# Optimization experiments

Measured on AMD Instinct MI355X. Metric: run time of the kernel, lower is better.

## Reference

```python
import jax, jax.numpy as jnp
import numpy as np

FLOW_NUM = 2048
H = 64  # lstm_output_dim
NOISE_DIM = 3


def _w(key, shape, s=0.08):
    return (jax.random.normal(key, shape, dtype=jnp.float32) * s)


def setup_inputs() -> dict:
    key = jax.random.key(0)
    ks = jax.random.split(key, 20)
    d = {
        "noise": jax.random.normal(ks[0], (FLOW_NUM, NOISE_DIM), dtype=jnp.float32),
        "w_ih0": _w(ks[1], (4 * H, NOISE_DIM)),
        "w_hh0": _w(ks[2], (4 * H, H)),
        "b_ih0": _w(ks[3], (4 * H,)),
        "b_hh0": _w(ks[4], (4 * H,)),
        "w_ih1": _w(ks[5], (4 * H, H)),
        "w_hh1": _w(ks[6], (4 * H, H)),
        "b_ih1": _w(ks[7], (4 * H,)),
        "b_hh1": _w(ks[8], (4 * H,)),
        "w_ih2": _w(ks[9], (4 * H, H)),
        "w_hh2": _w(ks[10], (4 * H, H)),
        "b_ih2": _w(ks[11], (4 * H,)),
        "b_hh2": _w(ks[12], (4 * H,)),
        "fc1_w": _w(ks[13], (32, H)),
        "fc1_b": _w(ks[14], (32,)),
        "fc2_w": _w(ks[15], (16, 32)),
        "fc2_b": _w(ks[16], (16,)),
        "fc3_w": _w(ks[17], (3, 16)),
        "fc3_b": _w(ks[18], (3,)),
        "flow_length": 500,
    }
    return d


def _lstm_cell(x, h, c, w_ih, w_hh, b_ih, b_hh):
    # PyTorch gate order: input, forget, cell(g), output
    gates = x @ w_ih.T + h @ w_hh.T + (b_ih + b_hh)
    i, f, g, o = jnp.split(gates, 4, axis=-1)
    c_new = jax.nn.sigmoid(f) * c + jax.nn.sigmoid(i) * jnp.tanh(g)
    h_new = jax.nn.sigmoid(o) * jnp.tanh(c_new)
    return h_new, c_new


def reference(noise, w_ih0, w_hh0, b_ih0, b_hh0,
              w_ih1, w_hh1, b_ih1, b_hh1,
              w_ih2, w_hh2, b_ih2, b_hh2,
              fc1_w, fc1_b, fc2_w, fc2_b, fc3_w, fc3_b,
              flow_length):
    layers = [(w_ih0, w_hh0, b_ih0, b_hh0),
              (w_ih1, w_hh1, b_ih1, b_hh1),
              (w_ih2, w_hh2, b_ih2, b_hh2)]
    n = noise.shape[0]
    h0 = jnp.zeros((3, n, H), dtype=noise.dtype)
    c0 = jnp.zeros((3, n, H), dtype=noise.dtype)

    def step(carry, _):
        x, h, c = carry
        inp = x
        hs, cs = [], []
        for l, (wi, wh, bi, bh) in enumerate(layers):
            h_l, c_l = _lstm_cell(inp, h[l], c[l], wi, wh, bi, bh)
            hs.append(h_l)
            cs.append(c_l)
            inp = h_l
        # MLP head (Dropout is identity in eval mode); LeakyReLU slope 0.01
        y = jax.nn.leaky_relu(inp @ fc1_w.T + fc1_b)
        y = jax.nn.leaky_relu(y @ fc2_w.T + fc2_b)
        y = jax.nn.leaky_relu(y @ fc3_w.T + fc3_b)
        return (y, jnp.stack(hs), jnp.stack(cs)), y

    _, flow = jax.lax.scan(step, (noise, h0, c0), None, length=flow_length)
    # flow: [flow_length, flow_num, 3] -> [flow_num, flow_length, 3]
    return jnp.swapaxes(flow, 0, 1)
```

## Files before the change

### kernel.cpp

```cpp
#include <hip/hip_runtime.h>

#define NT 512

typedef _Float16 f16x8 __attribute__((ext_vector_type(8)));
typedef float    f32x4 __attribute__((ext_vector_type(4)));
typedef unsigned u32x4 __attribute__((ext_vector_type(4)));

#define MFMA(a, b, c) __builtin_amdgcn_mfma_f32_16x16x32_f16((a), (b), (c), 0, 0, 0)

#if __has_builtin(__builtin_amdgcn_exp2f)
__device__ __forceinline__ float fexp(float x) { return __builtin_amdgcn_exp2f(x * 1.4426950408889634f); }
#else
__device__ __forceinline__ float fexp(float x) { return __expf(x); }
#endif
#if __has_builtin(__builtin_amdgcn_rcpf)
__device__ __forceinline__ float frcp(float x) { return __builtin_amdgcn_rcpf(x); }
#else
__device__ __forceinline__ float frcp(float x) { return 1.0f / x; }
#endif
__device__ __forceinline__ float sigm(float x)  { return frcp(1.0f + fexp(-x)); }
__device__ __forceinline__ float tanh_(float x) { return 1.0f - 2.0f * frcp(1.0f + fexp(2.0f * x)); }
__device__ __forceinline__ float lrelu(float x) { return x > 0.0f ? x : 0.01f * x; }

__device__ __forceinline__ f16x8 ld8(const float* p) {
    const float4* q = (const float4*)p;
    float4 a = q[0], b = q[1];
    f16x8 r = { (_Float16)a.x, (_Float16)a.y, (_Float16)a.z, (_Float16)a.w,
                (_Float16)b.x, (_Float16)b.y, (_Float16)b.z, (_Float16)b.w };
    return r;
}

__device__ __forceinline__ unsigned pkh(float a, float b) {
    auto h = __builtin_amdgcn_cvt_pkrtz(a, b);
    return __builtin_bit_cast(unsigned, h);
}
__device__ __forceinline__ unsigned shflu(unsigned v, int lane) {
    return (unsigned)__shfl((int)v, lane, 64);
}

__global__ __launch_bounds__(NT, 2)
void gen_kernel(
    const float* __restrict__ noise,
    const float* __restrict__ w_ih0, const float* __restrict__ w_hh0,
    const float* __restrict__ b_ih0, const float* __restrict__ b_hh0,
    const float* __restrict__ w_ih1, const float* __restrict__ w_hh1,
    const float* __restrict__ b_ih1, const float* __restrict__ b_hh1,
    const float* __restrict__ w_ih2, const float* __restrict__ w_hh2,
    const float* __restrict__ b_ih2, const float* __restrict__ b_hh2,
    const float* __restrict__ fc1_w, const float* __restrict__ fc1_b,
    const float* __restrict__ fc2_w, const float* __restrict__ fc2_b,
    const float* __restrict__ fc3_w, const float* __restrict__ fc3_b,
    const int*   __restrict__ flow_len_p,
    float* __restrict__ out)
{
    __shared__ _Float16 sh[3][2][16 * 64] __attribute__((aligned(16)));
    __shared__ _Float16 sx [16][40] __attribute__((aligned(16)));
    __shared__ float so[2][8][16][3] __attribute__((aligned(16)));

    const int tid  = threadIdx.x;
    const int l    = tid & 63;
    const int w    = tid >> 6;
    const int ls   = l & 15;
    const int lj   = l >> 4;
    const int base = blockIdx.x * 8;
    const int T    = flow_len_p[0];

    const int gA  = ls & 3;
    const int rA0 = gA * 64 + 4 * (2 * w + 0) + (ls >> 2);
    const int rA1 = gA * 64 + 4 * (2 * w + 1) + (ls >> 2);

    f16x8 A1[2][4], A2[2][4], A0[2][3];
#pragma unroll
    for (int kc = 0; kc < 2; ++kc) {
        A1[0][kc]     = ld8(w_ih1 + rA0 * 64 + 32 * kc + 8 * lj);
        A1[1][kc]     = ld8(w_ih1 + rA1 * 64 + 32 * kc + 8 * lj);
        A1[0][2 + kc] = ld8(w_hh1 + rA0 * 64 + 32 * kc + 8 * lj);
        A1[1][2 + kc] = ld8(w_hh1 + rA1 * 64 + 32 * kc + 8 * lj);
        A2[0][kc]     = ld8(w_ih2 + rA0 * 64 + 32 * kc + 8 * lj);
        A2[1][kc]     = ld8(w_ih2 + rA1 * 64 + 32 * kc + 8 * lj);
        A2[0][2 + kc] = ld8(w_hh2 + rA0 * 64 + 32 * kc + 8 * lj);
        A2[1][2 + kc] = ld8(w_hh2 + rA1 * 64 + 32 * kc + 8 * lj);
        A0[0][kc]     = ld8(w_hh0 + rA0 * 64 + 32 * kc + 8 * lj);
        A0[1][kc]     = ld8(w_hh0 + rA1 * 64 + 32 * kc + 8 * lj);
    }
#pragma unroll
    for (int tt = 0; tt < 2; ++tt) {
        const int r = tt ? rA1 : rA0;
        f16x8 v;
#pragma unroll
        for (int i = 0; i < 8; ++i) {
            int kl = 8 * lj + i;
            float x = (kl < 3) ? w_ih0[r * 3 + kl]
                    : (kl == 3) ? (b_ih0[r] + b_hh0[r]) : 0.0f;
            v[i] = (_Float16)x;
        }
        A0[tt][2] = v;
    }
    f16x8 F1[2][2], F2, F3;
#pragma unroll
    for (int tt = 0; tt < 2; ++tt)
#pragma unroll
        for (int kc = 0; kc < 2; ++kc)
            F1[tt][kc] = ld8(fc1_w + (16 * tt + ls) * 64 + 32 * kc + 8 * lj);
    F2 = ld8(fc2_w + ls * 32 + 8 * lj);
    {
        f16x8 v;
#pragma unroll
        for (int i = 0; i < 8; ++i) {
            int k = 8 * lj + i;
            v[i] = (_Float16)((ls < 3 && k < 16) ? fc3_w[ls * 16 + k] : 0.0f);
        }
        F3 = v;
    }
    const int uc0 = 8 * w + lj, uc1 = 8 * w + 4 + lj;
    const int u_own = (ls < 8) ? uc0 : uc1;
    const int cs    = ls & 7;
    const int whaddr = cs * 64 + 8 * (((u_own >> 3) + cs) & 7) + (u_own & 7);
    float b1o[4], b2o[4];
#pragma unroll
    for (int g = 0; g < 4; ++g) {
        b1o[g] = b_ih1[g * 64 + u_own] + b_hh1[g * 64 + u_own];
        b2o[g] = b_ih2[g * 64 + u_own] + b_hh2[g * 64 + u_own];
    }
    float hb1a[4], hb1b[4], hb2[4];
#pragma unroll
    for (int r = 0; r < 4; ++r) {
        hb1a[r] = fc1_b[4 * lj + r];
        hb1b[r] = fc1_b[16 + 4 * lj + r];
        hb2[r]  = fc2_b[4 * lj + r];
    }
    float fb3[3] = { fc3_b[0], fc3_b[1], fc3_b[2] };

    const int s01 = ls + 16 * ((2 * lj) & 3);
    const int s23 = ls + 16 * ((2 * lj + 1) & 3);

    for (int i = tid; i < 3 * 2 * 16 * 64; i += NT) ((_Float16*)sh)[i] = (_Float16)0.0f;
    for (int i = tid; i < 16 * 40; i += NT) ((_Float16*)sx)[i] = (_Float16)0.0f;
    __syncthreads();
    if (tid < 16) sx[tid][3] = (_Float16)1.0f;
    if (tid < 24) {
        int s = tid / 3, d = tid % 3;
        sx[s][d] = (_Float16)noise[(base + s) * 3 + d];
    }

    float c0s = 0.0f, c1s = 0.0f, c2s = 0.0f;
    const float zb[4] = {0, 0, 0, 0};
    const f32x4 z4 = {0, 0, 0, 0};
    __syncthreads();

#define RD(L, p, kg) (*(const f16x8*)&sh[L][p][ls * 64 + 8 * (((kg) + ls) & 7)])

#define REPACK(cell, a0, a1)                                                   \
    float cell[4];                                                             \
    _Pragma("unroll")                                                          \
    for (int r = 0; r < 4; ++r) {                                              \
        float v_ = __shfl_xor(a1[r], 8);                                       \
        cell[r] = (ls < 8) ? a0[r] : v_;                                       \
    }

#define ACTC(cell, bo, cref, L, p) {                                           \
        float gi = cell[0] + bo[0], gf = cell[1] + bo[1];                      \
        float gg = cell[2] + bo[2], go = cell[3] + bo[3];                      \
        cref = sigm(gf) * cref + sigm(gi) * tanh_(gg);                         \
        sh[L][p][whaddr] = (_Float16)(sigm(go) * tanh_(cref)); }

    {
        f16x8 bx = *(const f16x8*)&sx[ls][8 * lj];
        f32x4 a0 = z4, a1 = z4;
        a0 = MFMA(A0[0][2], bx, a0);
        a1 = MFMA(A0[1][2], bx, a1);
        REPACK(cell, a0, a1)
        ACTC(cell, zb, c0s, 0, 0)
    }
    __syncthreads();

    f32x4 u0 = z4, u1 = z4, p0 = z4, p1 = z4;

    for (int t = 0; t < T; ++t) {
        const int pc = t & 1, pp = pc ^ 1;
        f16x8 r0 = RD(0, pc, lj), r1 = RD(0, pc, 4 + lj);
        {
            f32x4 v0 = z4, v1 = z4;
            v0 = MFMA(A1[0][0], r0, v0);   v1 = MFMA(A1[1][0], r0, v1);
            v0 = MFMA(A1[0][1], r1, v0);   v1 = MFMA(A1[1][1], r1, v1);
            f32x4 a0 = u0 + v0, a1 = u1 + v1;
            REPACK(cell, a0, a1)
            ACTC(cell, b1o, c1s, 1, pc)
        }
        __syncthreads();
        f16x8 s0 = RD(1, pc, lj), s1 = RD(1, pc, 4 + lj);
        {
            f32x4 q0 = z4, q1 = z4;
            q0 = MFMA(A2[0][0], s0, q0);   q1 = MFMA(A2[1][0], s0, q1);
            q0 = MFMA(A2[0][1], s1, q0);   q1 = MFMA(A2[1][1], s1, q1);
            f32x4 a0 = p0 + q0, a1 = p1 + q1;
            REPACK(cell, a0, a1)
            ACTC(cell, b2o, c2s, 2, pc)
        }
        __syncthreads();
        f16x8 nh2a = RD(2, pc, lj), nh2b = RD(2, pc, 4 + lj);
        f32x4 h0a = z4, h0b = z4;
        h0a = MFMA(A0[0][0], r0, h0a); h0b = MFMA(A0[1][0], r0, h0b);
        h0a = MFMA(A0[0][1], r1, h0a); h0b = MFMA(A0[1][1], r1, h0b);
        p0 = MFMA(A2[0][2], nh2a, z4); p1 = MFMA(A2[1][2], nh2a, z4);
        p0 = MFMA(A2[0][3], nh2b, p0); p1 = MFMA(A2[1][3], nh2b, p1);
        if (w == 0) {
            f32x4 y1a = z4, y1b = z4;
            y1a = MFMA(F1[0][0], nh2a, y1a); y1b = MFMA(F1[1][0], nh2a, y1b);
            y1a = MFMA(F1[0][1], nh2b, y1a); y1b = MFMA(F1[1][1], nh2b, y1b);
            unsigned pa0 = pkh(lrelu(y1a[0] + hb1a[0]), lrelu(y1a[1] + hb1a[1]));
            unsigned pa1 = pkh(lrelu(y1a[2] + hb1a[2]), lrelu(y1a[3] + hb1a[3]));
            unsigned pb0 = pkh(lrelu(y1b[0] + hb1b[0]), lrelu(y1b[1] + hb1b[1]));
            unsigned pb1 = pkh(lrelu(y1b[2] + hb1b[2]), lrelu(y1b[3] + hb1b[3]));
            unsigned t0a = shflu(pa0, s01), t0b = shflu(pb0, s01);
            unsigned t1a = shflu(pa1, s01), t1b = shflu(pb1, s01);
            unsigned t2a = shflu(pa0, s23), t2b = shflu(pb0, s23);
            unsigned t3a = shflu(pa1, s23), t3b = shflu(pb1, s23);
            const bool lo = (lj < 2);
            u32x4 B1 = { lo ? t0a : t0b, lo ? t1a : t1b, lo ? t2a : t2b, lo ? t3a : t3b };
            f16x8 by1 = __builtin_bit_cast(f16x8, B1);
            f32x4 y2 = z4;
            y2 = MFMA(F2, by1, y2);
            unsigned q0 = pkh(lrelu(y2[0] + hb2[0]), lrelu(y2[1] + hb2[1]));
            unsigned q1 = pkh(lrelu(y2[2] + hb2[2]), lrelu(y2[3] + hb2[3]));
            unsigned z0 = shflu(q0, s01), z1 = shflu(q1, s01);
            unsigned z2 = shflu(q0, s23), z3 = shflu(q1, s23);
            u32x4 B2 = { z0, z1, z2, z3 };
            f16x8 by2 = __builtin_bit_cast(f16x8, B2);
            f32x4 y3 = z4;
            y3 = MFMA(F3, by2, y3);
            if (lj == 0) {
                float o0 = lrelu(y3[0] + fb3[0]);
                float o1 = lrelu(y3[1] + fb3[1]);
                float o2 = lrelu(y3[2] + fb3[2]);
                sx[ls][0] = (_Float16)o0;
                sx[ls][1] = (_Float16)o1;
                sx[ls][2] = (_Float16)o2;
                if (ls < 8) {
                    float* sp = &so[(t >> 4) & 1][ls][t & 15][0];
                    sp[0] = o0; sp[1] = o1; sp[2] = o2;
                }
            }
        }
        if (w == 7 && t >= 16 && (t & 15) == 0) {
            const int tb = t - 16, pb = (tb >> 4) & 1;
            for (int task = l; task < 96; task += 64) {
                int s = task / 12, c = task % 12;
                *(float4*)(out + ((size_t)(base + s) * T + tb) * 3 + 4 * c) =
                    *(const float4*)((const float*)&so[pb][s][0][0] + 4 * c);
            }
        }
        __syncthreads();
        {
            f16x8 bx = *(const f16x8*)&sx[ls][8 * lj];
            u0 = MFMA(A1[0][2], s0, z4); u1 = MFMA(A1[1][2], s0, z4);
            u0 = MFMA(A1[0][3], s1, u0); u1 = MFMA(A1[1][3], s1, u1);
            h0a = MFMA(A0[0][2], bx, h0a);
            h0b = MFMA(A0[1][2], bx, h0b);
            REPACK(cell, h0a, h0b)
            ACTC(cell, zb, c0s, 0, pp)
        }
        __syncthreads();
    }

    if (w == 7 && T > 0) {
        const int tf = ((T - 1) >> 4) << 4;
        const int pb = (tf >> 4) & 1;
        const int n  = T - tf;
        for (int task = l; task < n * 8 * 3; task += 64) {
            int s = task / (n * 3), r = task % (n * 3);
            int q = r / 3, d = r % 3;
            out[((size_t)(base + s) * T + tf + q) * 3 + d] = so[pb][s][q][d];
        }
    }
}

extern "C" void kernel_launch(void* const* d_in, const int* in_sizes, int n_in,
                              void* d_out, int out_size, void* d_ws, size_t ws_size,
                              hipStream_t stream) {
    const float* noise = (const float*)d_in[0];
    const float* w_ih0 = (const float*)d_in[1];
    const float* w_hh0 = (const float*)d_in[2];
    const float* b_ih0 = (const float*)d_in[3];
    const float* b_hh0 = (const float*)d_in[4];
    const float* w_ih1 = (const float*)d_in[5];
    const float* w_hh1 = (const float*)d_in[6];
    const float* b_ih1 = (const float*)d_in[7];
    const float* b_hh1 = (const float*)d_in[8];
    const float* w_ih2 = (const float*)d_in[9];
    const float* w_hh2 = (const float*)d_in[10];
    const float* b_ih2 = (const float*)d_in[11];
    const float* b_hh2 = (const float*)d_in[12];
    const float* fc1w  = (const float*)d_in[13];
    const float* fc1b  = (const float*)d_in[14];
    const float* fc2w  = (const float*)d_in[15];
    const float* fc2b  = (const float*)d_in[16];
    const float* fc3w  = (const float*)d_in[17];
    const float* fc3b  = (const float*)d_in[18];
    const int*   flp   = (const int*)d_in[19];

    gen_kernel<<<dim3(256), dim3(NT), 0, stream>>>(
        noise, w_ih0, w_hh0, b_ih0, b_hh0,
        w_ih1, w_hh1, b_ih1, b_hh1,
        w_ih2, w_hh2, b_ih2, b_hh2,
        fc1w, fc1b, fc2w, fc2b, fc3w, fc3b,
        flp, (float*)d_out);
}
```

Baseline: 858.4 us.

## Move recurrent-h MFMAs into critical layer phases and prioritize MLP wave

Drops the precomputed partial sums (u, p) that were calculated off the critical path. Layers 1 and 2 now run their recurrent h@W_hh MFMAs inline, using h values read from shared memory earlier in the step. This lengthens the dependent chain inside each layer phase but frees accumulator registers. It also raises wave 0's scheduling priority while it computes the MLP head, to shorten the serial feedback path. The net effect depends on whether the register savings outweigh the longer critical path.

```diff
diff --git a/kernel.cpp b/kernel.cpp
--- a/kernel.cpp
+++ b/kernel.cpp
@@ -173,41 +173,42 @@
         ACTC(cell, zb, c0s, 0, 0)
     }
     __syncthreads();
-
-    f32x4 u0 = z4, u1 = z4, p0 = z4, p1 = z4;
+    f16x8 ph1a = RD(1, 1, lj), ph1b = RD(1, 1, 4 + lj);
 
     for (int t = 0; t < T; ++t) {
         const int pc = t & 1, pp = pc ^ 1;
         f16x8 r0 = RD(0, pc, lj), r1 = RD(0, pc, 4 + lj);
+        f16x8 nh2a = RD(2, pp, lj), nh2b = RD(2, pp, 4 + lj);
         {
-            f32x4 v0 = z4, v1 = z4;
-            v0 = MFMA(A1[0][0], r0, v0);   v1 = MFMA(A1[1][0], r0, v1);
-            v0 = MFMA(A1[0][1], r1, v0);   v1 = MFMA(A1[1][1], r1, v1);
-            f32x4 a0 = u0 + v0, a1 = u1 + v1;
+            f32x4 a0 = z4, a1 = z4;
+            a0 = MFMA(A1[0][0], r0, a0);   a1 = MFMA(A1[1][0], r0, a1);
+            a0 = MFMA(A1[0][1], r1, a0);   a1 = MFMA(A1[1][1], r1, a1);
+            a0 = MFMA(A1[0][2], ph1a, a0); a1 = MFMA(A1[1][2], ph1a, a1);
+            a0 = MFMA(A1[0][3], ph1b, a0); a1 = MFMA(A1[1][3], ph1b, a1);
             REPACK(cell, a0, a1)
             ACTC(cell, b1o, c1s, 1, pc)
         }
         __syncthreads();
-        f16x8 s0 = RD(1, pc, lj), s1 = RD(1, pc, 4 + lj);
         {
-            f32x4 q0 = z4, q1 = z4;
-            q0 = MFMA(A2[0][0], s0, q0);   q1 = MFMA(A2[1][0], s0, q1);
-            q0 = MFMA(A2[0][1], s1, q0);   q1 = MFMA(A2[1][1], s1, q1);
-            f32x4 a0 = p0 + q0, a1 = p1 + q1;
+            f16x8 s0 = RD(1, pc, lj), s1 = RD(1, pc, 4 + lj);
+            f32x4 a0 = z4, a1 = z4;
+            a0 = MFMA(A2[0][0], s0, a0);   a1 = MFMA(A2[1][0], s0, a1);
+            a0 = MFMA(A2[0][1], s1, a0);   a1 = MFMA(A2[1][1], s1, a1);
+            a0 = MFMA(A2[0][2], nh2a, a0); a1 = MFMA(A2[1][2], nh2a, a1);
+            a0 = MFMA(A2[0][3], nh2b, a0); a1 = MFMA(A2[1][3], nh2b, a1);
             REPACK(cell, a0, a1)
             ACTC(cell, b2o, c2s, 2, pc)
         }
         __syncthreads();
-        f16x8 nh2a = RD(2, pc, lj), nh2b = RD(2, pc, 4 + lj);
         f32x4 h0a = z4, h0b = z4;
         h0a = MFMA(A0[0][0], r0, h0a); h0b = MFMA(A0[1][0], r0, h0b);
         h0a = MFMA(A0[0][1], r1, h0a); h0b = MFMA(A0[1][1], r1, h0b);
-        p0 = MFMA(A2[0][2], nh2a, z4); p1 = MFMA(A2[1][2], nh2a, z4);
-        p0 = MFMA(A2[0][3], nh2b, p0); p1 = MFMA(A2[1][3], nh2b, p1);
         if (w == 0) {
+            __builtin_amdgcn_s_setprio(1);
+            f16x8 bh0 = RD(2, pc, lj), bh1 = RD(2, pc, 4 + lj);
             f32x4 y1a = z4, y1b = z4;
-            y1a = MFMA(F1[0][0], nh2a, y1a); y1b = MFMA(F1[1][0], nh2a, y1b);
-            y1a = MFMA(F1[0][1], nh2b, y1a); y1b = MFMA(F1[1][1], nh2b, y1b);
+            y1a = MFMA(F1[0][0], bh0, y1a); y1b = MFMA(F1[1][0], bh0, y1b);
+            y1a = MFMA(F1[0][1], bh1, y1a); y1b = MFMA(F1[1][1], bh1, y1b);
             unsigned pa0 = pkh(lrelu(y1a[0] + hb1a[0]), lrelu(y1a[1] + hb1a[1]));
             unsigned pa1 = pkh(lrelu(y1a[2] + hb1a[2]), lrelu(y1a[3] + hb1a[3]));
             unsigned pb0 = pkh(lrelu(y1b[0] + hb1b[0]), lrelu(y1b[1] + hb1b[1]));
@@ -241,6 +242,7 @@
                     sp[0] = o0; sp[1] = o1; sp[2] = o2;
                 }
             }
+            __builtin_amdgcn_s_setprio(0);
         }
         if (w == 7 && t >= 16 && (t & 15) == 0) {
             const int tb = t - 16, pb = (tb >> 4) & 1;
@@ -253,13 +255,12 @@
         __syncthreads();
         {
             f16x8 bx = *(const f16x8*)&sx[ls][8 * lj];
-            u0 = MFMA(A1[0][2], s0, z4); u1 = MFMA(A1[1][2], s0, z4);
-            u0 = MFMA(A1[0][3], s1, u0); u1 = MFMA(A1[1][3], s1, u1);
             h0a = MFMA(A0[0][2], bx, h0a);
             h0b = MFMA(A0[1][2], bx, h0b);
             REPACK(cell, h0a, h0b)
             ACTC(cell, zb, c0s, 0, pp)
         }
+        ph1a = RD(1, pc, lj); ph1b = RD(1, pc, 4 + lj);
         __syncthreads();
     }
 
```

Result: faster. 825.0 us (-3.9%).
